# Performance work log

Hardware: AMD Instinct MI355X
Metric: run time of the kernel (lower is better)

Reference implementation:

```python
import jax, jax.numpy as jnp
import numpy as np

EMBED_DIM = 256
NUM_HEADS = 8


def setup_inputs() -> dict:
    key = jax.random.key(0)
    k1, k2, k3, k4 = jax.random.split(key, 4)
    b, nq, h, w = 2, 900, 16, 16
    attn_scores = jax.random.normal(k1, (b, nq, nq), dtype=jnp.float32)
    reference_points = jax.random.normal(k2, (b, nq, h, w), dtype=jnp.float32)
    # topology_proj = Linear(1, embed) -> ReLU -> Linear(embed, num_heads)
    w1 = jax.random.normal(k3, (EMBED_DIM,), dtype=jnp.float32) / 1.0  # Linear(1,E) weight, shape [E,1] squeezed
    b1 = jnp.zeros((EMBED_DIM,), dtype=jnp.float32)
    w2 = jax.random.normal(k4, (EMBED_DIM, NUM_HEADS), dtype=jnp.float32) / np.sqrt(EMBED_DIM)
    b2 = jnp.zeros((NUM_HEADS,), dtype=jnp.float32)
    lam = jnp.float32(0.1)
    return {"attn_scores": attn_scores, "reference_points": reference_points,
            "lam": lam, "w1": w1, "b1": b1, "w2": w2, "b2": b2}


def _process_reference_points(ref_pts):
    # ref_pts: [b, nq, h, w] -> argmax location normalized to [0,1]
    b, nq, h, w = ref_pts.shape
    flat = ref_pts.reshape(b, nq, h * w)
    idx = jnp.argmax(flat, axis=-1)                      # [b, nq] int
    y = (idx // w).astype(jnp.float32) / (h - 1)
    x = (idx % w).astype(jnp.float32) / (w - 1)
    return jnp.stack([x, y], axis=-1)                    # [b, nq, 2]


def reference(attn_scores, reference_points, lam, w1, b1, w2, b2):
    centers = _process_reference_points(reference_points)          # [b, nq, 2]
    # pairwise euclidean distance (torch.cdist)
    diff = centers[:, :, None, :] - centers[:, None, :, :]          # [b, nq, nq, 2]
    dist = jnp.sqrt(jnp.sum(diff * diff, axis=-1))                  # [b, nq, nq]
    mean_dist = jnp.mean(dist, axis=(1, 2), keepdims=True)
    topology = dist / (mean_dist + 1e-6)                            # [b, nq, nq]
    # tiny MLP on scalar feature: Linear(1,E) -> ReLU -> Linear(E,H)
    hdn = jax.nn.relu(topology[..., None] * w1 + b1)                # [b, nq, nq, E]
    bias = jnp.einsum('bqke,eh->bqkh', hdn, w2) + b2                # [b, nq, nq, H]
    bias_mean = jnp.mean(bias, axis=-1)                             # mean over heads -> [b, nq, nq]
    return attn_scores + lam * bias_mean
```

## Files before the change

kernel.cpp:

```cpp
#include <hip/hip_runtime.h>


#define NQ    900
#define LUT_N 451

__global__ __launch_bounds__(256)
void k1_centers(const float* __restrict__ ref, int* __restrict__ ws) {
    __shared__ int ctmp[4];
    const int tid  = threadIdx.x;
    const int lane = tid & 63;
    const int wave = tid >> 6;
    const int q    = blockIdx.x * 4 + wave;

    const float4* p4 = (const float4*)(ref + (size_t)q * 256);
    float4 v = p4[lane];
    float bv = v.x; int bi = lane * 4;
    if (v.y > bv) { bv = v.y; bi = lane * 4 + 1; }
    if (v.z > bv) { bv = v.z; bi = lane * 4 + 2; }
    if (v.w > bv) { bv = v.w; bi = lane * 4 + 3; }
    #pragma unroll
    for (int off = 32; off >= 1; off >>= 1) {
        float ov = __shfl_down(bv, off, 64);
        int   oi = __shfl_down(bi, off, 64);
        if (ov > bv || (ov == bv && oi < bi)) { bv = ov; bi = oi; }
    }
    if (lane == 0) ctmp[wave] = bi;
    __syncthreads();
    if (tid == 0)
        ws[blockIdx.x] = (ctmp[0] & 255)        | ((ctmp[1] & 255) << 8) |
                         ((ctmp[2] & 255) << 16) | ((ctmp[3] & 255) << 24);
}

__global__ __launch_bounds__(256)
void k2_stats_apply(const float* __restrict__ attn,
                    const float* __restrict__ lam_p,
                    const float* __restrict__ w1,
                    const float* __restrict__ b1,
                    const float* __restrict__ w2,
                    const float* __restrict__ b2,
                    const int* __restrict__ ws,
                    float* __restrict__ out) {
    const int tid  = threadIdx.x;
    const int lane = tid & 63;
    const int wave = tid >> 6;
    const int b    = blockIdx.y;

    const float4* attn4 = (const float4*)attn;
    float4*       out4  = (float4*)out;
    const int f4l = blockIdx.x * 2048 + tid;
    float4 a[8];
    if (blockIdx.x < 98) {
        #pragma unroll
        for (int u = 0; u < 8; ++u)
            a[u] = attn4[(size_t)b * 202500 + f4l + u * 256];
    } else {
        #pragma unroll
        for (int u = 0; u < 8; ++u)
            if (f4l + u * 256 < 202500)
                a[u] = attn4[(size_t)b * 202500 + f4l + u * 256];
    }

    __shared__ int   cpk[225];
    __shared__ int   hsh[256];
    __shared__ float sqs[LUT_N];
    __shared__ float w1s[256], b1s[256], wbars[256];
    __shared__ float lut_s[LUT_N];
    __shared__ float wsum[4];

    if (tid < 225) cpk[tid] = ws[b * 225 + tid];
    hsh[tid] = 0;
    w1s[tid] = w1[tid];
    b1s[tid] = b1[tid];
    {
        float s8 = 0.f;
        #pragma unroll
        for (int h = 0; h < 8; ++h) s8 += w2[tid * 8 + h];
        wbars[tid] = s8 * 0.125f;
    }
    for (int s = tid; s < LUT_N; s += 256) sqs[s] = sqrtf((float)s);
    __syncthreads();

    for (int k = tid; k < NQ; k += 256) {
        int c = (cpk[k >> 2] >> ((k & 3) * 8)) & 255;
        atomicAdd(&hsh[c], 1);
    }
    __syncthreads();

    float local = 0.f;
    {
        int h2v = hsh[tid];
        if (h2v) {
            int ix2 = tid & 15, iy2 = tid >> 4;
            for (int c1 = 0; c1 < 256; ++c1) {
                int h1 = hsh[c1];
                int dx = (c1 & 15) - ix2;
                int dy = (c1 >> 4) - iy2;
                local += (float)h1 * sqs[dx * dx + dy * dy];
            }
            local *= (float)h2v;
        }
    }
    #pragma unroll
    for (int off = 32; off >= 1; off >>= 1) local += __shfl_down(local, off, 64);
    if (lane == 0) wsum[wave] = local;
    __syncthreads();

    float tot   = wsum[0] + wsum[1] + wsum[2] + wsum[3];
    float mean  = tot * (1.f / 15.f) * (1.f / ((float)NQ * (float)NQ));
    float inv   = 1.f / (mean + 1e-6f);
    float b2bar = 0.125f * (b2[0] + b2[1] + b2[2] + b2[3] +
                            b2[4] + b2[5] + b2[6] + b2[7]);
    float lam   = lam_p[0];

    {
        float t0   = sqs[tid] * (1.f / 15.f) * inv;
        bool  has1 = (tid + 256 < LUT_N);
        float t1   = has1 ? sqs[tid + 256] * (1.f / 15.f) * inv : 0.f;
        float acc0 = b2bar, acc1 = b2bar;
        for (int i = 0; i < 256; ++i) {
            float w  = w1s[i];
            float bb = b1s[i];
            float wb = wbars[i];
            float h0 = fmaf(t0, w, bb);
            acc0 = fmaf(fmaxf(h0, 0.f), wb, acc0);
            float h1 = fmaf(t1, w, bb);
            acc1 = fmaf(fmaxf(h1, 0.f), wb, acc1);
        }
        lut_s[tid] = lam * acc0;
        if (has1) lut_s[tid + 256] = lam * acc1;
    }
    __syncthreads();

    #pragma unroll
    for (int u = 0; u < 8; ++u) {
        int f4 = f4l + u * 256;
        if (f4 < 202500) {
            int i  = (int)((unsigned)f4 / 225u);
            int j4 = f4 - i * 225;
            int ci = (cpk[i >> 2] >> ((i & 3) * 8)) & 255;
            int ixi = ci & 15, iyi = ci >> 4;
            int cw = cpk[j4];
            float4 v = a[u];
            int c, dx, dy;
            c = cw & 255;         dx = ixi - (c & 15); dy = iyi - (c >> 4); v.x += lut_s[dx*dx + dy*dy];
            c = (cw >> 8) & 255;  dx = ixi - (c & 15); dy = iyi - (c >> 4); v.y += lut_s[dx*dx + dy*dy];
            c = (cw >> 16) & 255; dx = ixi - (c & 15); dy = iyi - (c >> 4); v.z += lut_s[dx*dx + dy*dy];
            c = (cw >> 24) & 255; dx = ixi - (c & 15); dy = iyi - (c >> 4); v.w += lut_s[dx*dx + dy*dy];
            out4[(size_t)b * 202500 + f4] = v;
        }
    }
}

extern "C" void kernel_launch(void* const* d_in, const int* in_sizes, int n_in,
                              void* d_out, int out_size, void* d_ws, size_t ws_size,
                              hipStream_t stream) {
    const float* attn = (const float*)d_in[0];
    const float* ref  = (const float*)d_in[1];
    const float* lam  = (const float*)d_in[2];
    const float* w1   = (const float*)d_in[3];
    const float* b1   = (const float*)d_in[4];
    const float* w2   = (const float*)d_in[5];
    const float* b2   = (const float*)d_in[6];
    float* out = (float*)d_out;
    int*   ws  = (int*)d_ws;

    k1_centers<<<450, 256, 0, stream>>>(ref, ws);
    k2_stats_apply<<<dim3(99, 2), 256, 0, stream>>>(attn, lam, w1, b1, w2, b2, ws, out);
}
```

Baseline: 85.56 us.

## Fuse argmax center computation into the stats/apply kernel

Removes the separate center-extraction kernel and the workspace round-trip. Each block recomputes the argmax for all queries of its batch, with each of 225 threads scanning four 256-element rows serially. This drops a launch and the inter-kernel dependency. In exchange, every block does redundant work and reads about 900 KB of ref, with strided, poorly coalesced per-thread loads.

```diff
diff --git a/kernel.cpp b/kernel.cpp
--- a/kernel.cpp
+++ b/kernel.cpp
@@ -4,42 +4,29 @@
 #define NQ    900
 #define LUT_N 451
 
-__global__ __launch_bounds__(256)
-void k1_centers(const float* __restrict__ ref, int* __restrict__ ws) {
-    __shared__ int ctmp[4];
-    const int tid  = threadIdx.x;
-    const int lane = tid & 63;
-    const int wave = tid >> 6;
-    const int q    = blockIdx.x * 4 + wave;
-
-    const float4* p4 = (const float4*)(ref + (size_t)q * 256);
-    float4 v = p4[lane];
-    float bv = v.x; int bi = lane * 4;
-    if (v.y > bv) { bv = v.y; bi = lane * 4 + 1; }
-    if (v.z > bv) { bv = v.z; bi = lane * 4 + 2; }
-    if (v.w > bv) { bv = v.w; bi = lane * 4 + 3; }
-    #pragma unroll
-    for (int off = 32; off >= 1; off >>= 1) {
-        float ov = __shfl_down(bv, off, 64);
-        int   oi = __shfl_down(bi, off, 64);
-        if (ov > bv || (ov == bv && oi < bi)) { bv = ov; bi = oi; }
+#define ARGSTEP(V, BV, BI, K)                                               \
+    {                                                                       \
+        float m01_ = fmaxf((V).x, (V).y);                                   \
+        float m23_ = fmaxf((V).z, (V).w);                                   \
+        float m_   = fmaxf(m01_, m23_);                                     \
+        if (m_ > (BV)) {                                                    \
+            (BV) = m_;                                                      \
+            int kb_ = (K) * 4;                                              \
+            (BI) = ((V).x == m_) ? kb_                                      \
+                 : ((V).y == m_) ? kb_ + 1                                  \
+                 : ((V).z == m_) ? kb_ + 2 : kb_ + 3;                       \
+        }                                                                   \
     }
-    if (lane == 0) ctmp[wave] = bi;
-    __syncthreads();
-    if (tid == 0)
-        ws[blockIdx.x] = (ctmp[0] & 255)        | ((ctmp[1] & 255) << 8) |
-                         ((ctmp[2] & 255) << 16) | ((ctmp[3] & 255) << 24);
-}
 
 __global__ __launch_bounds__(256)
-void k2_stats_apply(const float* __restrict__ attn,
-                    const float* __restrict__ lam_p,
-                    const float* __restrict__ w1,
-                    const float* __restrict__ b1,
-                    const float* __restrict__ w2,
-                    const float* __restrict__ b2,
-                    const int* __restrict__ ws,
-                    float* __restrict__ out) {
+void k_fused(const float* __restrict__ attn,
+             const float* __restrict__ ref,
+             const float* __restrict__ lam_p,
+             const float* __restrict__ w1,
+             const float* __restrict__ b1,
+             const float* __restrict__ w2,
+             const float* __restrict__ b2,
+             float* __restrict__ out) {
     const int tid  = threadIdx.x;
     const int lane = tid & 63;
     const int wave = tid >> 6;
@@ -60,14 +47,13 @@
                 a[u] = attn4[(size_t)b * 202500 + f4l + u * 256];
     }
 
-    __shared__ int   cpk[225];
+    __shared__ int   cpk[226];
     __shared__ int   hsh[256];
     __shared__ float sqs[LUT_N];
     __shared__ float w1s[256], b1s[256], wbars[256];
     __shared__ float lut_s[LUT_N];
     __shared__ float wsum[4];
 
-    if (tid < 225) cpk[tid] = ws[b * 225 + tid];
     hsh[tid] = 0;
     w1s[tid] = w1[tid];
     b1s[tid] = b1[tid];
@@ -78,6 +64,26 @@
         wbars[tid] = s8 * 0.125f;
     }
     for (int s = tid; s < LUT_N; s += 256) sqs[s] = sqrtf((float)s);
+
+    if (tid < 225) {
+        const float*  rb = ref + ((size_t)b * 900 + (size_t)tid * 4) * 256;
+        const float4* r0 = (const float4*)(rb);
+        const float4* r1 = (const float4*)(rb + 256);
+        const float4* r2 = (const float4*)(rb + 512);
+        const float4* r3 = (const float4*)(rb + 768);
+        float bv0 = -1e38f, bv1 = -1e38f, bv2 = -1e38f, bv3 = -1e38f;
+        int   bi0 = 0, bi1 = 0, bi2 = 0, bi3 = 0;
+        #pragma unroll 4
+        for (int k = 0; k < 64; ++k) {
+            float4 v0 = r0[k], v1 = r1[k], v2 = r2[k], v3 = r3[k];
+            ARGSTEP(v0, bv0, bi0, k)
+            ARGSTEP(v1, bv1, bi1, k)
+            ARGSTEP(v2, bv2, bi2, k)
+            ARGSTEP(v3, bv3, bi3, k)
+        }
+        cpk[tid] = (bi0 & 255)        | ((bi1 & 255) << 8) |
+                   ((bi2 & 255) << 16) | ((bi3 & 255) << 24);
+    }
     __syncthreads();
 
     for (int k = tid; k < NQ; k += 256) {
@@ -162,8 +168,7 @@
     const float* w2   = (const float*)d_in[5];
     const float* b2   = (const float*)d_in[6];
     float* out = (float*)d_out;
-    int*   ws  = (int*)d_ws;
+    (void)d_ws; (void)ws_size;
 
-    k1_centers<<<450, 256, 0, stream>>>(ref, ws);
-    k2_stats_apply<<<dim3(99, 2), 256, 0, stream>>>(attn, lam, w1, b1, w2, b2, ws, out);
+    k_fused<<<dim3(99, 2), 256, 0, stream>>>(attn, ref, lam, w1, b1, w2, b2, out);
 }
```

Measured after the change: 133.2 us. +55.6%, slower.
